# Optimization experiments

Hardware: AMD Instinct MI355X
Metric: run time of the kernel (lower is better)

## Reference

```python
import jax, jax.numpy as jnp
import numpy as np

NEG_INF = -1000000.0  # matches torch masked_fill constant


def setup_inputs() -> dict:
    key = jax.random.key(0)
    k1, k2, k3, k4 = jax.random.split(key, 4)
    B, Lq, Lk, d = 64, 1024, 1024, 64
    queries = jax.random.normal(k1, (B, Lq, d), dtype=jnp.float32)
    keys = jax.random.normal(k2, (B, Lk, d), dtype=jnp.float32)
    values = jax.random.normal(k3, (B, Lk, d), dtype=jnp.float32)
    valid_lens = jax.random.randint(k4, (B,), 0, 1024, dtype=jnp.int64)
    return {"queries": queries, "keys": keys, "values": values, "valid_lens": valid_lens}


def reference(queries, keys, values, valid_lens):
    d = queries.shape[-1]
    # [B, Lq, Lk] scores
    scores = jnp.einsum("bqd,bkd->bqk", queries, keys) / jnp.sqrt(jnp.float32(d))
    Lk = scores.shape[-1]
    # valid_lens is per-batch (dim 1 in torch): same mask across all query rows
    mask = jnp.arange(Lk)[None, None, :] < valid_lens[:, None, None]  # [B,1,Lk]
    scores = jnp.where(mask, scores, NEG_INF)
    attn = jax.nn.softmax(scores, axis=-1)
    # dropout p=0.0 -> identity
    return jnp.einsum("bqk,bkd->bqd", attn, values)
```

## Files before the change

kernel.cpp:

```cpp
#include <hip/hip_runtime.h>
#include <hip/hip_bf16.h>

#define NEG_BIG -1000000.0f

typedef __attribute__((ext_vector_type(8))) short short8;
typedef __attribute__((ext_vector_type(4))) short short4v;
typedef __attribute__((ext_vector_type(4))) float floatx4;

#if __has_builtin(__builtin_amdgcn_exp2f)
#define EXP2F(x) __builtin_amdgcn_exp2f(x)
#else
#define EXP2F(x) exp2f(x)
#endif

#if __has_builtin(__builtin_amdgcn_mfma_f32_16x16x16bf16_1k)
#define MFMA16(a, b, c) __builtin_amdgcn_mfma_f32_16x16x16bf16_1k(a, b, c, 0, 0, 0)
#else
static __device__ __forceinline__ floatx4 MFMA16_fn(short4v a, short4v b, floatx4 c) {
    floatx4 d;
    asm("v_mfma_f32_16x16x16_bf16 %0, %1, %2, %3\n\ts_nop 4"
        : "=v"(d) : "v"(a), "v"(b), "v"(c));
    return d;
}
#define MFMA16(a, b, c) MFMA16_fn(a, b, c)
#endif

#if __has_builtin(__builtin_amdgcn_permlane16_swap) && __has_builtin(__builtin_amdgcn_permlane32_swap)
static __device__ __forceinline__ float redmax16_32(float x) {
    auto a = __builtin_amdgcn_permlane16_swap(__float_as_int(x), __float_as_int(x), false, false);
    x = fmaxf(__int_as_float(a[0]), __int_as_float(a[1]));
    auto b = __builtin_amdgcn_permlane32_swap(__float_as_int(x), __float_as_int(x), false, false);
    return fmaxf(__int_as_float(b[0]), __int_as_float(b[1]));
}
static __device__ __forceinline__ float redsum16_32(float x) {
    auto a = __builtin_amdgcn_permlane16_swap(__float_as_int(x), __float_as_int(x), false, false);
    x = __int_as_float(a[0]) + __int_as_float(a[1]);
    auto b = __builtin_amdgcn_permlane32_swap(__float_as_int(x), __float_as_int(x), false, false);
    return __int_as_float(b[0]) + __int_as_float(b[1]);
}
#else
static __device__ __forceinline__ float redmax16_32(float x) {
    x = fmaxf(x, __shfl_xor(x, 16));
    return fmaxf(x, __shfl_xor(x, 32));
}
static __device__ __forceinline__ float redsum16_32(float x) {
    x += __shfl_xor(x, 16);
    return x + __shfl_xor(x, 32);
}
#endif

static __device__ __forceinline__ unsigned short bf16u(float f) {
    union { __hip_bfloat16 h; unsigned short u; } c;
    c.h = __float2bfloat16(f);
    return c.u;
}

static __device__ __forceinline__ short8 pack8(float4 a, float4 b) {
    union { short8 s; __hip_bfloat162 h[4]; } u;
    u.h[0] = __float22bfloat162_rn(make_float2(a.x, a.y));
    u.h[1] = __float22bfloat162_rn(make_float2(a.z, a.w));
    u.h[2] = __float22bfloat162_rn(make_float2(b.x, b.y));
    u.h[3] = __float22bfloat162_rn(make_float2(b.z, b.w));
    return u.s;
}

__global__ __launch_bounds__(256, 4)
void attn_fwd(const float* __restrict__ Q, const float* __restrict__ K,
              const float* __restrict__ V, const int* __restrict__ vlen,
              float* __restrict__ out)
{
    __shared__ __attribute__((aligned(16))) unsigned short K_lds[2][4096];
    __shared__ __attribute__((aligned(16))) unsigned short VT_lds[2][4096];

    const int bid  = blockIdx.x;
    const int orig = (bid & 7) * 128 + (bid >> 3);
    const int b    = orig >> 4;
    const int qc   = orig & 15;

    const int tid = threadIdx.x;
    const int l   = tid & 63;
    const int w   = tid >> 6;
    const int lr  = l & 15;
    const int lg  = l >> 4;

    const float* Qb = Q + (size_t)b * 65536;
    const float* Kb = K + (size_t)b * 65536;
    const float* Vb = V + (size_t)b * 65536;

    const int valid = vlen[b];
    const int kmax  = (valid == 0) ? 1024 : valid;
    const int ntile = (kmax + 63) >> 6;

    const float qscale = 0.18033688011112042f;
    short8 qf[2];
#pragma unroll
    for (int c = 0; c < 2; ++c) {
        const float* p = Qb + (size_t)(qc*64 + w*16 + lr) * 64 + c*32 + lg*8;
        float4 a = *(const float4*)p, bb = *(const float4*)(p + 4);
        a.x *= qscale; a.y *= qscale; a.z *= qscale; a.w *= qscale;
        bb.x *= qscale; bb.y *= qscale; bb.z *= qscale; bb.w *= qscale;
        qf[c] = pack8(a, bb);
    }

    floatx4 o[4];
#pragma unroll
    for (int n = 0; n < 4; ++n) o[n] = (floatx4){0.f, 0.f, 0.f, 0.f};
    float m = -INFINITY, lsum = 0.f;

    const int row   = w * 16 + (l >> 2);
    const int cbase = (l & 3) * 16;

    float4 kra[4], vra[4];

#define LOAD_K(T) do {                                                      \
    const float* pk = Kb + (size_t)((T)*64 + row) * 64 + cbase;             \
    kra[0] = *(const float4*)pk;       kra[1] = *(const float4*)(pk + 4);   \
    kra[2] = *(const float4*)(pk + 8); kra[3] = *(const float4*)(pk + 12);  \
    } while (0)

#define LOAD_V(T) do {                                                      \
    const float* pv = Vb + (size_t)((T)*64 + row) * 64 + cbase;             \
    vra[0] = *(const float4*)pv;       vra[1] = *(const float4*)(pv + 4);   \
    vra[2] = *(const float4*)(pv + 8); vra[3] = *(const float4*)(pv + 12);  \
    } while (0)

#define WRITE_K(B) do {                                                     \
    const int _fk = (row & 7) * 8;                                          \
    *(short8*)&K_lds[B][row*64 + (cbase ^ _fk)]       = pack8(kra[0], kra[1]); \
    *(short8*)&K_lds[B][row*64 + ((cbase + 8) ^ _fk)] = pack8(kra[2], kra[3]); \
    } while (0)

#define WRITE_V(B) do {                                                     \
    _Pragma("unroll")                                                       \
    for (int j = 0; j < 16; ++j) {                                          \
        const int dv = cbase + j;                                           \
        const int fv = ((dv & 7) ^ (dv >> 3)) * 8;                          \
        VT_lds[B][dv*64 + (row ^ fv)] = bf16u(((const float*)&vra[j>>2])[j&3]); \
    } } while (0)

    LOAD_K(0);
    LOAD_V(0);
    WRITE_K(0);
    WRITE_V(0);
    __syncthreads();

    for (int t = 0; t < ntile; ++t) {
        const int cur = t & 1;
        const int nxt = cur ^ 1;
        const int k0  = t * 64;
        const bool pf = (t + 1 < ntile);

        if (pf) { LOAD_K(t + 1); LOAD_V(t + 1); }

        floatx4 sa[4];
        __builtin_amdgcn_s_setprio(1);
#pragma unroll
        for (int n = 0; n < 4; ++n) {
            const int kr = n*16 + lr;
            const int fk = (lr & 7) * 8;
            const short8 kf0 = *(const short8*)&K_lds[cur][kr*64 + ((lg*8)      ^ fk)];
            const short8 kf1 = *(const short8*)&K_lds[cur][kr*64 + ((32 + lg*8) ^ fk)];
            sa[n] = (floatx4){0.f, 0.f, 0.f, 0.f};
            sa[n] = __builtin_amdgcn_mfma_f32_16x16x32_bf16(kf0, qf[0], sa[n], 0, 0, 0);
            sa[n] = __builtin_amdgcn_mfma_f32_16x16x32_bf16(kf1, qf[1], sa[n], 0, 0, 0);
        }
        __builtin_amdgcn_s_setprio(0);

        if ((k0 + 64) > valid) {
            const int kb = k0 + lg*4;
#pragma unroll
            for (int n = 0; n < 4; ++n)
#pragma unroll
            for (int r = 0; r < 4; ++r)
                sa[n][r] = (kb + n*16 + r >= valid) ? NEG_BIG : sa[n][r];
        }

        float rmax = fmaxf(
            fmaxf(fmaxf(fmaxf(sa[0][0], sa[0][1]), fmaxf(sa[0][2], sa[0][3])),
                  fmaxf(fmaxf(sa[1][0], sa[1][1]), fmaxf(sa[1][2], sa[1][3]))),
            fmaxf(fmaxf(fmaxf(sa[2][0], sa[2][1]), fmaxf(sa[2][2], sa[2][3])),
                  fmaxf(fmaxf(sa[3][0], sa[3][1]), fmaxf(sa[3][2], sa[3][3]))));
        rmax = redmax16_32(rmax);

        if (!__all(rmax <= m + 11.0f)) {
            const float nm = fmaxf(m, rmax);
            const float sc = EXP2F(m - nm);
            m = nm;
            lsum *= sc;
            float sc_r[4];
#pragma unroll
            for (int r = 0; r < 4; ++r) sc_r[r] = __shfl(sc, lg*4 + r);
#pragma unroll
            for (int n = 0; n < 4; ++n)
#pragma unroll
            for (int r = 0; r < 4; ++r) o[n][r] *= sc_r[r];
        }

        float rs = 0.f;
#pragma unroll
        for (int n = 0; n < 4; ++n)
#pragma unroll
        for (int r = 0; r < 4; ++r) {
            sa[n][r] = EXP2F(sa[n][r] - m);
            rs += sa[n][r];
        }
        lsum += redsum16_32(rs);

        short4v pk[4];
#pragma unroll
        for (int n = 0; n < 4; ++n) {
            union { short4v s; __hip_bfloat162 h[2]; } u;
            u.h[0] = __float22bfloat162_rn(make_float2(sa[n][0], sa[n][1]));
            u.h[1] = __float22bfloat162_rn(make_float2(sa[n][2], sa[n][3]));
            pk[n] = u.s;
        }

        if (pf) WRITE_K(nxt);

        __builtin_amdgcn_s_setprio(1);
#pragma unroll
        for (int kc = 0; kc < 4; ++kc) {
#pragma unroll
            for (int n2 = 0; n2 < 4; ++n2) {
                const int dv = n2*16 + lr;
                const int fv = ((dv & 7) ^ (dv >> 3)) * 8;
                const short4v vf = *(const short4v*)&VT_lds[cur][dv*64 + ((kc*16 + lg*4) ^ fv)];
                o[n2] = MFMA16(pk[kc], vf, o[n2]);
            }
        }
        __builtin_amdgcn_s_setprio(0);

        if (pf) WRITE_V(nxt);
        __syncthreads();
    }

    const float inv = 1.0f / lsum;
    float inv_r[4];
#pragma unroll
    for (int r = 0; r < 4; ++r) inv_r[r] = __shfl(inv, lg*4 + r);

    float* Ob = out + (size_t)b * 65536;
#pragma unroll
    for (int n = 0; n < 4; ++n)
#pragma unroll
    for (int r = 0; r < 4; ++r) {
        const int q = qc*64 + w*16 + lg*4 + r;
        Ob[(size_t)q * 64 + n*16 + lr] = o[n][r] * inv_r[r];
    }
#undef LOAD_K
#undef LOAD_V
#undef WRITE_K
#undef WRITE_V
}

extern "C" void kernel_launch(void* const* d_in, const int* in_sizes, int n_in,
                              void* d_out, int out_size, void* d_ws, size_t ws_size,
                              hipStream_t stream) {
    (void)in_sizes; (void)n_in; (void)d_ws; (void)ws_size; (void)out_size;
    const float* Q  = (const float*)d_in[0];
    const float* K  = (const float*)d_in[1];
    const float* V  = (const float*)d_in[2];
    const int*   vl = (const int*)d_in[3];
    float* O = (float*)d_out;
    attn_fwd<<<dim3(1024), dim3(256), 0, stream>>>(Q, K, V, vl, O);
}
```

Measured before the change: 43.51 us.

## Software-pipeline QK of next tile with softmax/PV of previous tile

Restructures the main loop so each iteration computes the QK scores of tile t while doing softmax and PV for tile t-1, with V held in a triple-buffered LDS ring. The aim is to overlap MFMA work with the exp/reduction latency and let independent chains interleave. In exchange it raises LDS use (extra 8KB per block) and register pressure from the extra live score fragments, which may hurt occupancy at 4 blocks/SIMD launch bounds.

```diff
diff --git a/kernel.cpp b/kernel.cpp
--- a/kernel.cpp
+++ b/kernel.cpp
@@ -70,7 +70,7 @@
               float* __restrict__ out)
 {
     __shared__ __attribute__((aligned(16))) unsigned short K_lds[2][4096];
-    __shared__ __attribute__((aligned(16))) unsigned short VT_lds[2][4096];
+    __shared__ __attribute__((aligned(16))) unsigned short VT_lds[3][4096];
 
     const int bid  = blockIdx.x;
     const int orig = (bid & 7) * 128 + (bid >> 3);
@@ -113,15 +113,15 @@
     float4 kra[4], vra[4];
 
 #define LOAD_K(T) do {                                                      \
-    const float* pk = Kb + (size_t)((T)*64 + row) * 64 + cbase;             \
-    kra[0] = *(const float4*)pk;       kra[1] = *(const float4*)(pk + 4);   \
-    kra[2] = *(const float4*)(pk + 8); kra[3] = *(const float4*)(pk + 12);  \
+    const float* pk_ = Kb + (size_t)((T)*64 + row) * 64 + cbase;            \
+    kra[0] = *(const float4*)pk_;       kra[1] = *(const float4*)(pk_ + 4); \
+    kra[2] = *(const float4*)(pk_ + 8); kra[3] = *(const float4*)(pk_ + 12);\
     } while (0)
 
 #define LOAD_V(T) do {                                                      \
-    const float* pv = Vb + (size_t)((T)*64 + row) * 64 + cbase;             \
-    vra[0] = *(const float4*)pv;       vra[1] = *(const float4*)(pv + 4);   \
-    vra[2] = *(const float4*)(pv + 8); vra[3] = *(const float4*)(pv + 12);  \
+    const float* pv_ = Vb + (size_t)((T)*64 + row) * 64 + cbase;            \
+    vra[0] = *(const float4*)pv_;       vra[1] = *(const float4*)(pv_ + 4); \
+    vra[2] = *(const float4*)(pv_ + 8); vra[3] = *(const float4*)(pv_ + 12);\
     } while (0)
 
 #define WRITE_K(B) do {                                                     \
@@ -138,101 +138,114 @@
         VT_lds[B][dv*64 + (row ^ fv)] = bf16u(((const float*)&vra[j>>2])[j&3]); \
     } } while (0)
 
+#define QK_COMPUTE(SA, KBUF, T) do {                                        \
+    const int _k0 = (T) * 64;                                               \
+    __builtin_amdgcn_s_setprio(1);                                          \
+    _Pragma("unroll")                                                       \
+    for (int n = 0; n < 4; ++n) {                                           \
+        const int kr_ = n*16 + lr;                                          \
+        const int fk_ = (lr & 7) * 8;                                       \
+        const short8 kf0 = *(const short8*)&K_lds[KBUF][kr_*64 + ((lg*8)      ^ fk_)]; \
+        const short8 kf1 = *(const short8*)&K_lds[KBUF][kr_*64 + ((32 + lg*8) ^ fk_)]; \
+        SA[n] = (floatx4){0.f, 0.f, 0.f, 0.f};                              \
+        SA[n] = __builtin_amdgcn_mfma_f32_16x16x32_bf16(kf0, qf[0], SA[n], 0, 0, 0); \
+        SA[n] = __builtin_amdgcn_mfma_f32_16x16x32_bf16(kf1, qf[1], SA[n], 0, 0, 0); \
+    }                                                                       \
+    __builtin_amdgcn_s_setprio(0);                                          \
+    if ((_k0 + 64) > valid) {                                               \
+        const int kb_ = _k0 + lg*4;                                         \
+        _Pragma("unroll")                                                   \
+        for (int n = 0; n < 4; ++n)                                         \
+        _Pragma("unroll")                                                   \
+        for (int r = 0; r < 4; ++r)                                         \
+            SA[n][r] = (kb_ + n*16 + r >= valid) ? NEG_BIG : SA[n][r];      \
+    } } while (0)
+
+#define SOFTMAX_PV(SA, VBUF) do {                                           \
+    float rmax = fmaxf(                                                     \
+        fmaxf(fmaxf(fmaxf(SA[0][0], SA[0][1]), fmaxf(SA[0][2], SA[0][3])),  \
+              fmaxf(fmaxf(SA[1][0], SA[1][1]), fmaxf(SA[1][2], SA[1][3]))), \
+        fmaxf(fmaxf(fmaxf(SA[2][0], SA[2][1]), fmaxf(SA[2][2], SA[2][3])),  \
+              fmaxf(fmaxf(SA[3][0], SA[3][1]), fmaxf(SA[3][2], SA[3][3])))); \
+    rmax = redmax16_32(rmax);                                               \
+    if (!__all(rmax <= m + 11.0f)) {                                        \
+        const float nm_ = fmaxf(m, rmax);                                   \
+        const float sc_f = EXP2F(m - nm_);                                  \
+        m = nm_;                                                            \
+        lsum *= sc_f;                                                       \
+        float sc_r[4];                                                      \
+        _Pragma("unroll")                                                   \
+        for (int r = 0; r < 4; ++r) sc_r[r] = __shfl(sc_f, lg*4 + r);       \
+        _Pragma("unroll")                                                   \
+        for (int n = 0; n < 4; ++n)                                         \
+        _Pragma("unroll")                                                   \
+        for (int r = 0; r < 4; ++r) o[n][r] *= sc_r[r];                     \
+    }                                                                       \
+    float rs = 0.f;                                                         \
+    _Pragma("unroll")                                                       \
+    for (int n = 0; n < 4; ++n)                                             \
+    _Pragma("unroll")                                                       \
+    for (int r = 0; r < 4; ++r) {                                           \
+        SA[n][r] = EXP2F(SA[n][r] - m);                                     \
+        rs += SA[n][r];                                                     \
+    }                                                                       \
+    lsum += redsum16_32(rs);                                                \
+    short4v pkf[4];                                                         \
+    _Pragma("unroll")                                                       \
+    for (int n = 0; n < 4; ++n) {                                           \
+        union { short4v s; __hip_bfloat162 h[2]; } u;                       \
+        u.h[0] = __float22bfloat162_rn(make_float2(SA[n][0], SA[n][1]));    \
+        u.h[1] = __float22bfloat162_rn(make_float2(SA[n][2], SA[n][3]));    \
+        pkf[n] = u.s;                                                       \
+    }                                                                       \
+    __builtin_amdgcn_s_setprio(1);                                          \
+    _Pragma("unroll")                                                       \
+    for (int kc = 0; kc < 4; ++kc) {                                        \
+        _Pragma("unroll")                                                   \
+        for (int n2 = 0; n2 < 4; ++n2) {                                    \
+            const int dv_ = n2*16 + lr;                                     \
+            const int fv_ = ((dv_ & 7) ^ (dv_ >> 3)) * 8;                   \
+            const short4v vf = *(const short4v*)&VT_lds[VBUF][dv_*64 + ((kc*16 + lg*4) ^ fv_)]; \
+            o[n2] = MFMA16(pkf[kc], vf, o[n2]);                             \
+        }                                                                   \
+    }                                                                       \
+    __builtin_amdgcn_s_setprio(0);                                          \
+    } while (0)
+
     LOAD_K(0);
     LOAD_V(0);
     WRITE_K(0);
     WRITE_V(0);
     __syncthreads();
 
-    for (int t = 0; t < ntile; ++t) {
-        const int cur = t & 1;
-        const int nxt = cur ^ 1;
-        const int k0  = t * 64;
+    floatx4 sp[4];
+    if (ntile > 1) { LOAD_K(1); LOAD_V(1); }
+    QK_COMPUTE(sp, 0, 0);
+    if (ntile > 1) {
+        WRITE_K(1);
+        WRITE_V(1);
+        __syncthreads();
+    }
+
+    int vr = 0, vw = 2;
+    for (int t = 1; t < ntile; ++t) {
         const bool pf = (t + 1 < ntile);
-
         if (pf) { LOAD_K(t + 1); LOAD_V(t + 1); }
 
-        floatx4 sa[4];
-        __builtin_amdgcn_s_setprio(1);
-#pragma unroll
-        for (int n = 0; n < 4; ++n) {
-            const int kr = n*16 + lr;
-            const int fk = (lr & 7) * 8;
-            const short8 kf0 = *(const short8*)&K_lds[cur][kr*64 + ((lg*8)      ^ fk)];
-            const short8 kf1 = *(const short8*)&K_lds[cur][kr*64 + ((32 + lg*8) ^ fk)];
-            sa[n] = (floatx4){0.f, 0.f, 0.f, 0.f};
-            sa[n] = __builtin_amdgcn_mfma_f32_16x16x32_bf16(kf0, qf[0], sa[n], 0, 0, 0);
-            sa[n] = __builtin_amdgcn_mfma_f32_16x16x32_bf16(kf1, qf[1], sa[n], 0, 0, 0);
-        }
-        __builtin_amdgcn_s_setprio(0);
-
-        if ((k0 + 64) > valid) {
-            const int kb = k0 + lg*4;
-#pragma unroll
-            for (int n = 0; n < 4; ++n)
-#pragma unroll
-            for (int r = 0; r < 4; ++r)
-                sa[n][r] = (kb + n*16 + r >= valid) ? NEG_BIG : sa[n][r];
-        }
-
-        float rmax = fmaxf(
-            fmaxf(fmaxf(fmaxf(sa[0][0], sa[0][1]), fmaxf(sa[0][2], sa[0][3])),
-                  fmaxf(fmaxf(sa[1][0], sa[1][1]), fmaxf(sa[1][2], sa[1][3]))),
-            fmaxf(fmaxf(fmaxf(sa[2][0], sa[2][1]), fmaxf(sa[2][2], sa[2][3])),
-                  fmaxf(fmaxf(sa[3][0], sa[3][1]), fmaxf(sa[3][2], sa[3][3]))));
-        rmax = redmax16_32(rmax);
-
-        if (!__all(rmax <= m + 11.0f)) {
-            const float nm = fmaxf(m, rmax);
-            const float sc = EXP2F(m - nm);
-            m = nm;
-            lsum *= sc;
-            float sc_r[4];
-#pragma unroll
-            for (int r = 0; r < 4; ++r) sc_r[r] = __shfl(sc, lg*4 + r);
-#pragma unroll
-            for (int n = 0; n < 4; ++n)
-#pragma unroll
-            for (int r = 0; r < 4; ++r) o[n][r] *= sc_r[r];
-        }
-
-        float rs = 0.f;
-#pragma unroll
-        for (int n = 0; n < 4; ++n)
-#pragma unroll
-        for (int r = 0; r < 4; ++r) {
-            sa[n][r] = EXP2F(sa[n][r] - m);
-            rs += sa[n][r];
-        }
-        lsum += redsum16_32(rs);
-
-        short4v pk[4];
-#pragma unroll
-        for (int n = 0; n < 4; ++n) {
-            union { short4v s; __hip_bfloat162 h[2]; } u;
-            u.h[0] = __float22bfloat162_rn(make_float2(sa[n][0], sa[n][1]));
-            u.h[1] = __float22bfloat162_rn(make_float2(sa[n][2], sa[n][3]));
-            pk[n] = u.s;
-        }
-
-        if (pf) WRITE_K(nxt);
-
-        __builtin_amdgcn_s_setprio(1);
-#pragma unroll
-        for (int kc = 0; kc < 4; ++kc) {
-#pragma unroll
-            for (int n2 = 0; n2 < 4; ++n2) {
-                const int dv = n2*16 + lr;
-                const int fv = ((dv & 7) ^ (dv >> 3)) * 8;
-                const short4v vf = *(const short4v*)&VT_lds[cur][dv*64 + ((kc*16 + lg*4) ^ fv)];
-                o[n2] = MFMA16(pk[kc], vf, o[n2]);
-            }
-        }
-        __builtin_amdgcn_s_setprio(0);
-
-        if (pf) WRITE_V(nxt);
+        floatx4 sc[4];
+        QK_COMPUTE(sc, t & 1, t);
+        SOFTMAX_PV(sp, vr);
+
+        if (pf) { WRITE_K((t + 1) & 1); WRITE_V(vw); }
         __syncthreads();
-    }
+
+#pragma unroll
+        for (int n = 0; n < 4; ++n) sp[n] = sc[n];
+        vr = (vr == 2) ? 0 : vr + 1;
+        vw = (vw == 2) ? 0 : vw + 1;
+    }
+
+    SOFTMAX_PV(sp, vr);
 
     const float inv = 1.0f / lsum;
     float inv_r[4];
@@ -251,6 +264,8 @@
 #undef LOAD_V
 #undef WRITE_K
 #undef WRITE_V
+#undef QK_COMPUTE
+#undef SOFTMAX_PV
 }
 
 extern "C" void kernel_launch(void* const* d_in, const int* in_sizes, int n_in,
```

New measurement: 58.04 us. 33.4% more time.
